# Kernel optimization log

Hardware: AMD Instinct MI355X
Metric: run time of the kernel (lower is better)

The kernel has to match this reference:

```python
import jax, jax.numpy as jnp
import numpy as np

EPS = 1e-5
GROUPS = 16


def _deform_conv_gn(input, offset, mask, weight, bias, gamma, beta):
    # Modulated deformable conv v2 (k=3, stride=1, pad=1) + GroupNorm(16).
    B, C, H, W = input.shape
    Co = weight.shape[0]
    K = 9
    # kernel taps relative to center (pad=1 cancels the -1 origin shift)
    ky = jnp.repeat(jnp.arange(3) - 1, 3).astype(input.dtype)   # [9]
    kx = jnp.tile(jnp.arange(3) - 1, 3).astype(input.dtype)     # [9]
    off = offset.reshape(B, K, 2, H, W)                          # (dy, dx) per tap
    dy, dx = off[:, :, 0], off[:, :, 1]                          # [B,9,H,W]
    y = jnp.arange(H, dtype=input.dtype)[None, None, :, None] + ky[None, :, None, None] + dy
    x = jnp.arange(W, dtype=input.dtype)[None, None, None, :] + kx[None, :, None, None] + dx
    y0 = jnp.floor(y)
    x0 = jnp.floor(x)
    flat = input.reshape(B, C, H * W)

    def corner(yc, xc):
        # zero-padded bilinear corner gather -> [B,C,9,H,W]
        valid = ((yc >= 0) & (yc < H) & (xc >= 0) & (xc < W)).astype(input.dtype)
        yi = jnp.clip(yc, 0, H - 1).astype(jnp.int32)
        xi = jnp.clip(xc, 0, W - 1).astype(jnp.int32)
        idx = (yi * W + xi).reshape(B, -1)
        g = jax.vmap(lambda im, ix: jnp.take(im, ix, axis=1))(flat, idx)
        return g.reshape(B, C, K, H, W) * valid[:, None]

    wy1 = y - y0
    wx1 = x - x0
    wy0 = 1.0 - wy1
    wx0 = 1.0 - wx1
    val = (corner(y0, x0) * (wy0 * wx0)[:, None]
           + corner(y0, x0 + 1.0) * (wy0 * wx1)[:, None]
           + corner(y0 + 1.0, x0) * (wy1 * wx0)[:, None]
           + corner(y0 + 1.0, x0 + 1.0) * (wy1 * wx1)[:, None])
    cols = val * mask[:, None]                                   # modulation [B,C,9,H,W]
    out = jnp.einsum('bckhw,ock->bohw', cols, weight.reshape(Co, C, K))
    out = out + bias[None, :, None, None]
    # GroupNorm(16)
    g = out.reshape(B, GROUPS, Co // GROUPS, H, W)
    mu = g.mean(axis=(2, 3, 4), keepdims=True)
    var = g.var(axis=(2, 3, 4), keepdims=True)
    g = (g - mu) * jax.lax.rsqrt(var + EPS)
    return g.reshape(B, Co, H, W) * gamma[None, :, None, None] + beta[None, :, None, None]


def setup_inputs() -> dict:
    key = jax.random.key(0)
    k1, k2, k3, k4 = jax.random.split(key, 4)
    B, C, Co, H, W = 4, 256, 256, 64, 64
    return {
        'input': jax.random.normal(k1, (B, C, H, W), dtype=jnp.float32),
        'offset': jax.random.normal(k2, (B, 18, H, W), dtype=jnp.float32),
        'mask': jax.random.uniform(k3, (B, 9, H, W), dtype=jnp.float32),
        'weight': jax.random.normal(k4, (Co, C, 3, 3), dtype=jnp.float32) * 0.02,
        'bias': jnp.zeros((Co,), dtype=jnp.float32),
        'gamma': jnp.ones((Co,), dtype=jnp.float32),
        'beta': jnp.zeros((Co,), dtype=jnp.float32),
    }


def reference(input, offset, mask, weight, bias, gamma, beta):
    return _deform_conv_gn(input, offset, mask, weight, bias, gamma, beta)
```

## Files before the change

### kernel.cpp

```cpp
#include <hip/hip_runtime.h>

typedef __attribute__((ext_vector_type(8))) short short8;
typedef __attribute__((ext_vector_type(4))) float f32x4;

#define Bsz 4
#define Cin 256
#define Cout 256
#define Hh 64
#define Ww 64
#define HW 4096
#define NG 16
#define EPSV 1e-5f

#define SPAN 12
#define ROWB 4112

#define OFF_IN   0
#define SZ_IN    (SPAN * ROWB)
#define OFF_COL  49344
#define SZ_COL   (9 * 2048)
#define OFF_CTL  67776
#define SMEM_BYTES 67792

static __device__ __forceinline__ unsigned f2bf(float f) {
    unsigned u = __float_as_uint(f);
    return (u + 0x7fffu + ((u >> 16) & 1u)) >> 16;
}

static __device__ __forceinline__ float2 ld8(const float* p) {
    float2 v;
    __builtin_memcpy(&v, p, 8);
    return v;
}

#define BLO(u) __uint_as_float((u) << 16)
#define BHI(u) __uint_as_float((u) & 0xffff0000u)

__launch_bounds__(512)
__global__ void prep_kernel(const float* __restrict__ in,
                            const float* __restrict__ w,
                            unsigned* __restrict__ inT,
                            ushort* __restrict__ wtb,
                            float* __restrict__ stats) {
    const int t  = threadIdx.x;
    const int bx = blockIdx.x;
    if (bx < 256) {
        const int b = bx >> 6, y = bx & 63;
        const int x = t & 63, w8 = t >> 6;
        const float* src = in + (size_t)b * 256 * HW + y * 64 + x;
        unsigned* dst = inT + ((size_t)(b * 64 + y) * 128) * 64 + x;
#pragma unroll
        for (int it = 0; it < 16; it++) {
            const int pr = w8 + it * 8;
            const float a0 = src[(size_t)(2 * pr) * HW];
            const float a1 = src[(size_t)(2 * pr + 1) * HW];
            dst[(size_t)pr * 64] = f2bf(a0) | (f2bf(a1) << 16);
        }
        return;
    }
    if (bx == 256 && t < 128) stats[t] = 0.f;
    const int i = (bx - 256) * 512 + t;
    if (i >= 72 * 256 * 32) return;
    const int cl = i & 31;
    const int o  = (i >> 5) & 255;
    const int ks = i >> 13;
    const int c  = ((ks & 7) << 5) | cl;
    const int kk = ks >> 3;
    wtb[i] = (ushort)f2bf(w[((size_t)o * Cin + c) * 9 + kk]);
}

__launch_bounds__(512, 4)
__global__ void dcn_kernel(const float* __restrict__ in,
                           const unsigned* __restrict__ inT,
                           const float* __restrict__ offs,
                           const float* __restrict__ mask,
                           const ushort* __restrict__ wtb,
                           const float* __restrict__ bias,
                           float* __restrict__ out,
                           float* __restrict__ stats) {
    extern __shared__ char smem[];
    ushort* col  = (ushort*)(smem + OFF_COL);
    int*    s_ctl = (int*)(smem + OFF_CTL);

    const int t  = threadIdx.x;
    const int bx = blockIdx.x;
    const int q  = bx & 7, r = bx >> 3;
    const int b  = q >> 1;
    const int h  = ((q & 1) << 5) | (r >> 1);
    const int wb = (r & 1) << 5;
    const int lane = t & 63;
    const int wv   = t >> 6;
    const int quad = lane >> 4;
    const int l15  = lane & 15;
    const int px   = lane & 31;
    const int hi   = lane >> 5;
    const int proff = (2 * wv + hi) * 256;
    const int pp   = wb + px;
    const int cslot = ((px >> 4) << 9) | ((wv >> 1) << 7) | ((px & 15) << 3) |
                      ((wv & 1) << 2) | (hi << 1);

    if (t < 2) s_ctl[t] = (t == 0) ? 64 : -1;
    __syncthreads();

    const float* ob = offs + (size_t)b * 18 * HW + h * Ww + pp;
    const float* mb = mask + (size_t)b * 9 * HW + h * Ww + pp;
    int ryc0[9], ryc1[9], rxb[9];
    float4 tw4[9];
    int my_min = 64, my_max = -1;
#pragma unroll
    for (int k = 0; k < 9; k++) {
        const float dy = ob[(2 * k) * HW];
        const float dx = ob[(2 * k + 1) * HW];
        const float m  = mb[k * HW];
        const float y = (float)h + (float)(k / 3 - 1) + dy;
        const float x = (float)pp + (float)(k % 3 - 1) + dx;
        const float y0f = floorf(y), x0f = floorf(x);
        const float ly = y - y0f, lx = x - x0f;
        const float hy = 1.f - ly, hx = 1.f - lx;
        const int y0 = (int)y0f, x0 = (int)x0f;
        const int yc0 = min(max(y0, 0), 63);
        const int yc1 = min(max(y0 + 1, 0), 63);
        const int xb  = min(max(x0, 0), 62);
        float ax = 0.f, ay = 0.f;
        if (x0 == xb) {
            ax = hx;
            ay = lx;
        } else if (x0 < xb) {
            ax = (x0 + 1 == 0) ? lx : 0.f;
        } else {
            ay = (x0 == 63) ? hx : 0.f;
        }
        const float w0 = (y0 >= 0 && y0 < 64) ? m * hy : 0.f;
        const float w1 = (y0 + 1 >= 0 && y0 + 1 < 64) ? m * ly : 0.f;
        ryc0[k] = yc0; ryc1[k] = yc1; rxb[k] = xb;
        tw4[k] = make_float4(w0 * ax, w0 * ay, w1 * ax, w1 * ay);
        my_min = min(my_min, yc0);
        my_max = max(my_max, yc1);
    }
#pragma unroll
    for (int off = 32; off; off >>= 1) {
        my_min = min(my_min, __shfl_xor(my_min, off));
        my_max = max(my_max, __shfl_xor(my_max, off));
    }
    if (lane == 0) {
        atomicMin(&s_ctl[0], my_min);
        atomicMax(&s_ctl[1], my_max);
    }
    __syncthreads();

    const int ymin = s_ctl[0];
    const bool use_lds = (s_ctl[1] - ymin + 1) <= SPAN;

    unsigned tad[9];
#pragma unroll
    for (int k = 0; k < 9; k++) {
        const unsigned r0 = (unsigned)((ryc0[k] - ymin) * ROWB + rxb[k] * 4);
        const unsigned r1 = (unsigned)((ryc1[k] - ymin) * ROWB + rxb[k] * 4);
        tad[k] = (r0 & 0xffffu) | (r1 << 16);
    }

    f32x4 acc[2][2];
#pragma unroll
    for (int i = 0; i < 2; i++)
#pragma unroll
        for (int nt = 0; nt < 2; nt++) acc[i][nt] = (f32x4){0.f, 0.f, 0.f, 0.f};

    const float* inb = in + (size_t)b * Cin * HW;

#define STAGE(cc)                                                              \
    {                                                                          \
        _Pragma("unroll")                                                      \
        for (int i = 0; i < 6; i++) {                                          \
            const int g = wv * 6 + i;                                          \
            const int rr = g >> 2, seg = g & 3;                                \
            const int row = min(ymin + rr, 63);                                \
            const unsigned* src = inT +                                        \
                ((size_t)(b * 64 + row) * 128 + (cc) * 16) * 64 +              \
                seg * 256 + lane * 4;                                          \
            __builtin_amdgcn_global_load_lds(                                  \
                (const __attribute__((address_space(1))) void*)src,            \
                (__attribute__((address_space(3))) void*)(smem + OFF_IN +      \
                    rr * ROWB + seg * 1024),                                   \
                16, 0, 0);                                                     \
        }                                                                      \
    }

#define GATHER_PUB_L(kk)                                                   \
    {                                                                      \
        const unsigned ad = tad[kk];                                       \
        const float4 tw = tw4[kk];                                         \
        const char* bp = smem + OFF_IN + proff;                            \
        const float2 f0 = ld8((const float*)(bp + (ad & 0xffffu)));        \
        const float2 f1 = ld8((const float*)(bp + (ad >> 16)));            \
        const unsigned u00 = __float_as_uint(f0.x);                        \
        const unsigned u01 = __float_as_uint(f0.y);                        \
        const unsigned u10 = __float_as_uint(f1.x);                        \
        const unsigned u11 = __float_as_uint(f1.y);                        \
        const float v0 = tw.x * BLO(u00) + tw.y * BLO(u01) +               \
                         tw.z * BLO(u10) + tw.w * BLO(u11);                \
        const float v1 = tw.x * BHI(u00) + tw.y * BHI(u01) +               \
                         tw.z * BHI(u10) + tw.w * BHI(u11);                \
        *(unsigned*)&col[(kk) * 1024 + cslot] = f2bf(v0) | (f2bf(v1) << 16); \
    }

#define FRAGS_MFMA(ks, kk)                                                     \
    {                                                                          \
        const ushort* wp =                                                     \
            wtb + ((size_t)((ks) * 256 + wv * 32 + l15)) * 32 + quad * 8;      \
        const short8 a0 = *(const short8*)wp;                                  \
        const short8 a1 = *(const short8*)(wp + 16 * 32);                      \
        short8 bfr[2];                                                         \
        _Pragma("unroll")                                                      \
        for (int nt = 0; nt < 2; nt++)                                         \
            bfr[nt] = *(const short8*)&col[(kk) * 1024 + nt * 512 +            \
                                           quad * 128 + l15 * 8];              \
        _Pragma("unroll")                                                      \
        for (int nt = 0; nt < 2; nt++) {                                       \
            acc[0][nt] = __builtin_amdgcn_mfma_f32_16x16x32_bf16(              \
                a0, bfr[nt], acc[0][nt], 0, 0, 0);                             \
            acc[1][nt] = __builtin_amdgcn_mfma_f32_16x16x32_bf16(              \
                a1, bfr[nt], acc[1][nt], 0, 0, 0);                             \
        }                                                                      \
    }

    if (use_lds) {
        STAGE(0);
        __syncthreads();
#pragma unroll 1
        for (int cc = 0; cc < 8; cc++) {
#pragma unroll
            for (int kk = 0; kk < 9; kk++) GATHER_PUB_L(kk);
            __syncthreads();
            if (cc < 7) STAGE(cc + 1);
#pragma unroll 3
            for (int kk = 0; kk < 9; kk++) FRAGS_MFMA(kk * 8 + cc, kk);
            __syncthreads();
        }
    } else {
#pragma unroll 1
        for (int cc = 0; cc < 8; cc++) {
#pragma unroll 1
            for (int kk = 0; kk < 9; kk++) {
                const float dy = ob[(2 * kk) * HW];
                const float dx = ob[(2 * kk + 1) * HW];
                const float m  = mb[kk * HW];
                const float y = (float)h + (float)(kk / 3 - 1) + dy;
                const float x = (float)pp + (float)(kk % 3 - 1) + dx;
                const float y0f = floorf(y), x0f = floorf(x);
                const float ly = y - y0f, lx = x - x0f;
                const float hy = 1.f - ly, hx = 1.f - lx;
                const int y0 = (int)y0f, x0 = (int)x0f;
                const int yc0 = min(max(y0, 0), 63);
                const int yc1 = min(max(y0 + 1, 0), 63);
                const int xb  = min(max(x0, 0), 62);
                float ax = 0.f, ay = 0.f;
                if (x0 == xb)      { ax = hx; ay = lx; }
                else if (x0 < xb)  { ax = (x0 + 1 == 0) ? lx : 0.f; }
                else               { ay = (x0 == 63) ? hx : 0.f; }
                const float w0 = (y0 >= 0 && y0 < 64) ? m * hy : 0.f;
                const float w1 = (y0 + 1 >= 0 && y0 + 1 < 64) ? m * ly : 0.f;
                const int adx = yc0 * 64 + xb, ady = yc1 * 64 + xb;
                const float* cb = inb + (size_t)(cc * 32 + wv * 4 + hi * 2) * HW;
                float vv[2];
#pragma unroll
                for (int j = 0; j < 2; j++) {
                    const float* pl = cb + j * HW;
                    const float2 g0 = ld8(pl + adx);
                    const float2 g1 = ld8(pl + ady);
                    vv[j] = (w0 * ax) * g0.x + (w0 * ay) * g0.y +
                            (w1 * ax) * g1.x + (w1 * ay) * g1.y;
                }
                *(unsigned*)&col[kk * 1024 + cslot] =
                    f2bf(vv[0]) | (f2bf(vv[1]) << 16);
            }
            __syncthreads();
#pragma unroll 3
            for (int kk = 0; kk < 9; kk++) FRAGS_MFMA(kk * 8 + cc, kk);
            __syncthreads();
        }
    }
#undef STAGE
#undef GATHER_PUB_L
#undef FRAGS_MFMA

    float gs[2], gq[2];
#pragma unroll
    for (int i = 0; i < 2; i++) {
        float s = 0.f, qq = 0.f;
        const int ob2 = wv * 32 + i * 16 + quad * 4;
#pragma unroll
        for (int reg = 0; reg < 4; reg++) {
            const int o = ob2 + reg;
            const float bv = bias[o];
            float* op = out + ((size_t)(b * 256 + o)) * HW + h * Ww + wb + l15;
#pragma unroll
            for (int nt = 0; nt < 2; nt++) {
                const float v = acc[i][nt][reg] + bv;
                op[nt * 16] = v;
                s += v;
                qq += v * v;
            }
        }
        gs[i] = s; gq[i] = qq;
    }
#pragma unroll
    for (int off = 32; off; off >>= 1) {
        gs[0] += __shfl_xor(gs[0], off);
        gq[0] += __shfl_xor(gq[0], off);
        gs[1] += __shfl_xor(gs[1], off);
        gq[1] += __shfl_xor(gq[1], off);
    }
    if (lane == 0) {
#pragma unroll
        for (int i = 0; i < 2; i++) {
            const int g = wv * 2 + i;
            atomicAdd(&stats[((size_t)b * NG + g) * 2],     gs[i]);
            atomicAdd(&stats[((size_t)b * NG + g) * 2 + 1], gq[i]);
        }
    }
}

__global__ void gn_apply_kernel(float* __restrict__ x, const float* __restrict__ stats,
                                const float* __restrict__ gamma,
                                const float* __restrict__ beta) {
    const int i = blockIdx.x * 256 + threadIdx.x;
    const int plane = i >> 10;
    const int o = plane & 255;
    const int bg = plane >> 4;
    const float s = stats[bg * 2], q = stats[bg * 2 + 1];
    const float inv_n = 1.f / 65536.f;
    const float mu = s * inv_n;
    const float var = q * inv_n - mu * mu;
    const float rs = rsqrtf(var + EPSV);
    const float ga = gamma[o] * rs;
    const float be = beta[o] - mu * ga;
    float4 v = ((float4*)x)[i];
    v.x = v.x * ga + be;
    v.y = v.y * ga + be;
    v.z = v.z * ga + be;
    v.w = v.w * ga + be;
    ((float4*)x)[i] = v;
}

extern "C" void kernel_launch(void* const* d_in, const int* in_sizes, int n_in,
                              void* d_out, int out_size, void* d_ws, size_t ws_size,
                              hipStream_t stream) {
    const float* input  = (const float*)d_in[0];
    const float* offset = (const float*)d_in[1];
    const float* maskp  = (const float*)d_in[2];
    const float* weight = (const float*)d_in[3];
    const float* bias   = (const float*)d_in[4];
    const float* gamma  = (const float*)d_in[5];
    const float* beta   = (const float*)d_in[6];
    float* out = (float*)d_out;

    ushort* wtb  = (ushort*)d_ws;
    float* stats = (float*)((char*)d_ws + (size_t)Cout * Cin * 9 * sizeof(ushort));
    unsigned* inT = (unsigned*)((char*)d_ws + 1180160);

    static int attr_done = 0;
    if (!attr_done) {
        hipFuncSetAttribute((const void*)dcn_kernel,
                            hipFuncAttributeMaxDynamicSharedMemorySize, SMEM_BYTES);
        attr_done = 1;
    }

    hipLaunchKernelGGL(prep_kernel, dim3(256 + 1152), dim3(512), 0, stream,
                       input, weight, inT, wtb, stats);
    hipLaunchKernelGGL(dcn_kernel, dim3(Bsz * Hh * 2), dim3(512), SMEM_BYTES, stream,
                       input, inT, offset, maskp, wtb, bias, out, stats);
    hipLaunchKernelGGL(gn_apply_kernel, dim3((Bsz * Cout * HW / 4) / 256), dim3(256), 0,
                       stream, out, stats, gamma, beta);
}
```

Baseline: 195.4 us.

## Fuse prep, deformable conv and GroupNorm into one cooperative grid-synced kernel

Replaces the three launches (prep transpose/weight conversion, DCN+stats, GN apply) with a single cooperative kernel of 512 blocks that uses grid-wide syncs between phases. The conv results are kept in registers so GroupNorm is applied without writing and re-reading the pre-norm output. This removes two launch gaps and one full round trip of the output through global memory. In exchange it adds grid barriers, requires all blocks to be co-resident (launch bounds of 4 blocks per CU), and may put register pressure on the accumulator path. It falls back to the old three-kernel path if cooperative launch is unavailable.

New measurement: 196.1 us. No clear change (+0.4%).

```diff
diff --git a/kernel.cpp b/kernel.cpp
--- a/kernel.cpp
+++ b/kernel.cpp
@@ -1,4 +1,7 @@
 #include <hip/hip_runtime.h>
+#include <hip/hip_cooperative_groups.h>
+
+namespace cg = cooperative_groups;
 
 typedef __attribute__((ext_vector_type(8))) short short8;
 typedef __attribute__((ext_vector_type(4))) float f32x4;
@@ -35,6 +38,305 @@
 
 #define BLO(u) __uint_as_float((u) << 16)
 #define BHI(u) __uint_as_float((u) & 0xffff0000u)
+
+#define STAGE(cc)                                                              \
+    {                                                                          \
+        _Pragma("unroll")                                                      \
+        for (int i = 0; i < 6; i++) {                                          \
+            const int g = wv * 6 + i;                                          \
+            const int rr = g >> 2, seg = g & 3;                                \
+            const int row = min(ymin + rr, 63);                                \
+            const unsigned* src = inT +                                        \
+                ((size_t)(b * 64 + row) * 128 + (cc) * 16) * 64 +              \
+                seg * 256 + lane * 4;                                          \
+            __builtin_amdgcn_global_load_lds(                                  \
+                (const __attribute__((address_space(1))) void*)src,            \
+                (__attribute__((address_space(3))) void*)(smem + OFF_IN +      \
+                    rr * ROWB + seg * 1024),                                   \
+                16, 0, 0);                                                     \
+        }                                                                      \
+    }
+
+#define GATHER_PUB_L(kk)                                                   \
+    {                                                                      \
+        const unsigned ad = tad[kk];                                       \
+        const float4 tw = tw4[kk];                                         \
+        const char* bp = smem + OFF_IN + proff;                            \
+        const float2 f0 = ld8((const float*)(bp + (ad & 0xffffu)));        \
+        const float2 f1 = ld8((const float*)(bp + (ad >> 16)));            \
+        const unsigned u00 = __float_as_uint(f0.x);                        \
+        const unsigned u01 = __float_as_uint(f0.y);                        \
+        const unsigned u10 = __float_as_uint(f1.x);                        \
+        const unsigned u11 = __float_as_uint(f1.y);                        \
+        const float v0 = tw.x * BLO(u00) + tw.y * BLO(u01) +               \
+                         tw.z * BLO(u10) + tw.w * BLO(u11);                \
+        const float v1 = tw.x * BHI(u00) + tw.y * BHI(u01) +               \
+                         tw.z * BHI(u10) + tw.w * BHI(u11);                \
+        *(unsigned*)&col[(kk) * 1024 + cslot] = f2bf(v0) | (f2bf(v1) << 16); \
+    }
+
+#define FRAGS_MFMA(ks, kk)                                                     \
+    {                                                                          \
+        const ushort* wp =                                                     \
+            wtb + ((size_t)((ks) * 256 + wv * 32 + l15)) * 32 + quad * 8;      \
+        const short8 a0 = *(const short8*)wp;                                  \
+        const short8 a1 = *(const short8*)(wp + 16 * 32);                      \
+        short8 bfr[2];                                                         \
+        _Pragma("unroll")                                                      \
+        for (int nt = 0; nt < 2; nt++)                                         \
+            bfr[nt] = *(const short8*)&col[(kk) * 1024 + nt * 512 +            \
+                                           quad * 128 + l15 * 8];              \
+        _Pragma("unroll")                                                      \
+        for (int nt = 0; nt < 2; nt++) {                                       \
+            acc[0][nt] = __builtin_amdgcn_mfma_f32_16x16x32_bf16(              \
+                a0, bfr[nt], acc[0][nt], 0, 0, 0);                             \
+            acc[1][nt] = __builtin_amdgcn_mfma_f32_16x16x32_bf16(              \
+                a1, bfr[nt], acc[1][nt], 0, 0, 0);                             \
+        }                                                                      \
+    }
+
+#define DCN_BODY(WRITE_OUT)                                                    \
+    if (t < 2) s_ctl[t] = (t == 0) ? 64 : -1;                                  \
+    __syncthreads();                                                           \
+    const float* ob = offs + (size_t)b * 18 * HW + h * Ww + pp;                \
+    const float* mb = mask + (size_t)b * 9 * HW + h * Ww + pp;                 \
+    int ryc0[9], ryc1[9], rxb[9];                                              \
+    float4 tw4[9];                                                             \
+    int my_min = 64, my_max = -1;                                              \
+    _Pragma("unroll")                                                          \
+    for (int k = 0; k < 9; k++) {                                              \
+        const float dy = ob[(2 * k) * HW];                                     \
+        const float dx = ob[(2 * k + 1) * HW];                                 \
+        const float m  = mb[k * HW];                                           \
+        const float y = (float)h + (float)(k / 3 - 1) + dy;                    \
+        const float x = (float)pp + (float)(k % 3 - 1) + dx;                   \
+        const float y0f = floorf(y), x0f = floorf(x);                          \
+        const float ly = y - y0f, lx = x - x0f;                                \
+        const float hy = 1.f - ly, hx = 1.f - lx;                              \
+        const int y0 = (int)y0f, x0 = (int)x0f;                                \
+        const int yc0 = min(max(y0, 0), 63);                                   \
+        const int yc1 = min(max(y0 + 1, 0), 63);                               \
+        const int xb  = min(max(x0, 0), 62);                                   \
+        float ax = 0.f, ay = 0.f;                                              \
+        if (x0 == xb)      { ax = hx; ay = lx; }                               \
+        else if (x0 < xb)  { ax = (x0 + 1 == 0) ? lx : 0.f; }                  \
+        else               { ay = (x0 == 63) ? hx : 0.f; }                     \
+        const float w0 = (y0 >= 0 && y0 < 64) ? m * hy : 0.f;                  \
+        const float w1 = (y0 + 1 >= 0 && y0 + 1 < 64) ? m * ly : 0.f;          \
+        ryc0[k] = yc0; ryc1[k] = yc1; rxb[k] = xb;                             \
+        tw4[k] = make_float4(w0 * ax, w0 * ay, w1 * ax, w1 * ay);              \
+        my_min = min(my_min, yc0);                                             \
+        my_max = max(my_max, yc1);                                             \
+    }                                                                          \
+    _Pragma("unroll")                                                          \
+    for (int off = 32; off; off >>= 1) {                                       \
+        my_min = min(my_min, __shfl_xor(my_min, off));                         \
+        my_max = max(my_max, __shfl_xor(my_max, off));                         \
+    }                                                                          \
+    if (lane == 0) {                                                           \
+        atomicMin(&s_ctl[0], my_min);                                          \
+        atomicMax(&s_ctl[1], my_max);                                          \
+    }                                                                          \
+    __syncthreads();                                                           \
+    const int ymin = s_ctl[0];                                                 \
+    const bool use_lds2 = (s_ctl[1] - ymin + 1) <= SPAN;                       \
+    unsigned tad[9];                                                           \
+    _Pragma("unroll")                                                          \
+    for (int k = 0; k < 9; k++) {                                              \
+        const unsigned r0 = (unsigned)((ryc0[k] - ymin) * ROWB + rxb[k] * 4);  \
+        const unsigned r1 = (unsigned)((ryc1[k] - ymin) * ROWB + rxb[k] * 4);  \
+        tad[k] = (r0 & 0xffffu) | (r1 << 16);                                  \
+    }                                                                          \
+    f32x4 acc[2][2];                                                           \
+    _Pragma("unroll")                                                          \
+    for (int i = 0; i < 2; i++)                                                \
+        _Pragma("unroll")                                                      \
+        for (int nt = 0; nt < 2; nt++) acc[i][nt] = (f32x4){0.f,0.f,0.f,0.f};  \
+    const float* inb = in + (size_t)b * Cin * HW;                              \
+    if (use_lds2) {                                                            \
+        STAGE(0);                                                              \
+        __syncthreads();                                                       \
+        _Pragma("unroll 1")                                                    \
+        for (int cc = 0; cc < 8; cc++) {                                       \
+            _Pragma("unroll")                                                  \
+            for (int kk = 0; kk < 9; kk++) GATHER_PUB_L(kk);                   \
+            __syncthreads();                                                   \
+            if (cc < 7) STAGE(cc + 1);                                         \
+            _Pragma("unroll 3")                                                \
+            for (int kk = 0; kk < 9; kk++) FRAGS_MFMA(kk * 8 + cc, kk);        \
+            __syncthreads();                                                   \
+        }                                                                      \
+    } else {                                                                   \
+        _Pragma("unroll 1")                                                    \
+        for (int cc = 0; cc < 8; cc++) {                                       \
+            _Pragma("unroll 1")                                                \
+            for (int kk = 0; kk < 9; kk++) {                                   \
+                const float dy = ob[(2 * kk) * HW];                            \
+                const float dx = ob[(2 * kk + 1) * HW];                        \
+                const float m  = mb[kk * HW];                                  \
+                const float y = (float)h + (float)(kk / 3 - 1) + dy;           \
+                const float x = (float)pp + (float)(kk % 3 - 1) + dx;          \
+                const float y0f = floorf(y), x0f = floorf(x);                  \
+                const float ly = y - y0f, lx = x - x0f;                        \
+                const float hy = 1.f - ly, hx = 1.f - lx;                      \
+                const int y0 = (int)y0f, x0 = (int)x0f;                        \
+                const int yc0 = min(max(y0, 0), 63);                           \
+                const int yc1 = min(max(y0 + 1, 0), 63);                       \
+                const int xb  = min(max(x0, 0), 62);                           \
+                float ax = 0.f, ay = 0.f;                                      \
+                if (x0 == xb)      { ax = hx; ay = lx; }                       \
+                else if (x0 < xb)  { ax = (x0 + 1 == 0) ? lx : 0.f; }          \
+                else               { ay = (x0 == 63) ? hx : 0.f; }             \
+                const float w0 = (y0 >= 0 && y0 < 64) ? m * hy : 0.f;          \
+                const float w1 = (y0 + 1 >= 0 && y0 + 1 < 64) ? m * ly : 0.f;  \
+                const int adx = yc0 * 64 + xb, ady = yc1 * 64 + xb;            \
+                const float* cb = inb + (size_t)(cc*32 + wv*4 + hi*2) * HW;    \
+                float vv[2];                                                   \
+                _Pragma("unroll")                                              \
+                for (int j = 0; j < 2; j++) {                                  \
+                    const float* pl = cb + j * HW;                             \
+                    const float2 g0 = ld8(pl + adx);                           \
+                    const float2 g1 = ld8(pl + ady);                           \
+                    vv[j] = (w0 * ax) * g0.x + (w0 * ay) * g0.y +              \
+                            (w1 * ax) * g1.x + (w1 * ay) * g1.y;               \
+                }                                                              \
+                *(unsigned*)&col[kk * 1024 + cslot] =                          \
+                    f2bf(vv[0]) | (f2bf(vv[1]) << 16);                         \
+            }                                                                  \
+            __syncthreads();                                                   \
+            _Pragma("unroll 3")                                                \
+            for (int kk = 0; kk < 9; kk++) FRAGS_MFMA(kk * 8 + cc, kk);        \
+            __syncthreads();                                                   \
+        }                                                                      \
+    }                                                                          \
+    float gs[2], gq[2];                                                        \
+    _Pragma("unroll")                                                          \
+    for (int i = 0; i < 2; i++) {                                              \
+        float s = 0.f, qq = 0.f;                                               \
+        const int ob2 = wv * 32 + i * 16 + quad * 4;                           \
+        _Pragma("unroll")                                                      \
+        for (int reg = 0; reg < 4; reg++) {                                    \
+            const int o = ob2 + reg;                                           \
+            const float bv = bias[o];                                          \
+            float* op = out + ((size_t)(b * 256 + o)) * HW + h * Ww + wb + l15;\
+            _Pragma("unroll")                                                  \
+            for (int nt = 0; nt < 2; nt++) {                                   \
+                const float v = acc[i][nt][reg] + bv;                          \
+                acc[i][nt][reg] = v;                                           \
+                if (WRITE_OUT) op[nt * 16] = v;                                \
+                s += v;                                                        \
+                qq += v * v;                                                   \
+            }                                                                  \
+        }                                                                      \
+        gs[i] = s; gq[i] = qq;                                                 \
+    }                                                                          \
+    _Pragma("unroll")                                                          \
+    for (int off = 32; off; off >>= 1) {                                       \
+        gs[0] += __shfl_xor(gs[0], off);                                       \
+        gq[0] += __shfl_xor(gq[0], off);                                       \
+        gs[1] += __shfl_xor(gs[1], off);                                       \
+        gq[1] += __shfl_xor(gq[1], off);                                       \
+    }                                                                          \
+    if (lane == 0) {                                                           \
+        _Pragma("unroll")                                                      \
+        for (int i = 0; i < 2; i++) {                                          \
+            const int g = wv * 2 + i;                                          \
+            atomicAdd(&stats[((size_t)b * NG + g) * 2],     gs[i]);            \
+            atomicAdd(&stats[((size_t)b * NG + g) * 2 + 1], gq[i]);            \
+        }                                                                      \
+    }
+
+__launch_bounds__(512, 4)
+__global__ void fused_kernel(const float* __restrict__ in,
+                             const float* __restrict__ offs,
+                             const float* __restrict__ mask,
+                             const float* __restrict__ w,
+                             const float* __restrict__ bias,
+                             const float* __restrict__ gamma,
+                             const float* __restrict__ beta,
+                             float* __restrict__ out,
+                             unsigned* __restrict__ inT,
+                             ushort* __restrict__ wtb,
+                             float* __restrict__ stats) {
+    extern __shared__ char smem[];
+    ushort* col  = (ushort*)(smem + OFF_COL);
+    int*    s_ctl = (int*)(smem + OFF_CTL);
+
+    const int t  = threadIdx.x;
+    const int bx = blockIdx.x;
+
+    {
+        const int pb = bx >> 7;
+        const int py = (bx >> 1) & 63;
+        const int ph = bx & 1;
+        const int x = t & 63, w8 = t >> 6;
+        const float* src = in + (size_t)pb * 256 * HW + py * 64 + x;
+        unsigned* dst = inT + ((size_t)(pb * 64 + py) * 128) * 64 + x;
+#pragma unroll
+        for (int it = 0; it < 8; it++) {
+            const int pr = ph * 64 + w8 + it * 8;
+            const float a0 = src[(size_t)(2 * pr) * HW];
+            const float a1 = src[(size_t)(2 * pr + 1) * HW];
+            dst[(size_t)pr * 64] = f2bf(a0) | (f2bf(a1) << 16);
+        }
+#pragma unroll
+        for (int j = 0; j < 3; j++) {
+            const int l = j * 512 + t;
+            if (l < 1152) {
+                const int i = bx * 1152 + l;
+                const int cl = i & 31;
+                const int o  = (i >> 5) & 255;
+                const int ks = i >> 13;
+                const int c  = ((ks & 7) << 5) | cl;
+                const int kk = ks >> 3;
+                wtb[i] = (ushort)f2bf(w[((size_t)o * Cin + c) * 9 + kk]);
+            }
+        }
+        if (bx == 0 && t < 128) stats[t] = 0.f;
+    }
+    cg::this_grid().sync();
+
+    const int q  = bx & 7, r = bx >> 3;
+    const int b  = q >> 1;
+    const int h  = ((q & 1) << 5) | (r >> 1);
+    const int wb = (r & 1) << 5;
+    const int lane = t & 63;
+    const int wv   = t >> 6;
+    const int quad = lane >> 4;
+    const int l15  = lane & 15;
+    const int px   = lane & 31;
+    const int hi   = lane >> 5;
+    const int proff = (2 * wv + hi) * 256;
+    const int pp   = wb + px;
+    const int cslot = ((px >> 4) << 9) | ((wv >> 1) << 7) | ((px & 15) << 3) |
+                      ((wv & 1) << 2) | (hi << 1);
+
+    DCN_BODY(0)
+
+    cg::this_grid().sync();
+
+    const float inv_n = 1.f / 65536.f;
+#pragma unroll
+    for (int i = 0; i < 2; i++) {
+        const int g = wv * 2 + i;
+        const float ssum = stats[((size_t)b * NG + g) * 2];
+        const float sq   = stats[((size_t)b * NG + g) * 2 + 1];
+        const float mu  = ssum * inv_n;
+        const float var = sq * inv_n - mu * mu;
+        const float rs  = rsqrtf(var + EPSV);
+        const int ob2 = wv * 32 + i * 16 + quad * 4;
+#pragma unroll
+        for (int reg = 0; reg < 4; reg++) {
+            const int o = ob2 + reg;
+            const float ga = gamma[o] * rs;
+            const float be = beta[o] - mu * ga;
+            float* op = out + ((size_t)(b * 256 + o)) * HW + h * Ww + wb + l15;
+#pragma unroll
+            for (int nt = 0; nt < 2; nt++)
+                op[nt * 16] = acc[i][nt][reg] * ga + be;
+        }
+    }
+}
 
 __launch_bounds__(512)
 __global__ void prep_kernel(const float* __restrict__ in,
@@ -99,226 +401,13 @@
     const int cslot = ((px >> 4) << 9) | ((wv >> 1) << 7) | ((px & 15) << 3) |
                       ((wv & 1) << 2) | (hi << 1);
 
-    if (t < 2) s_ctl[t] = (t == 0) ? 64 : -1;
-    __syncthreads();
-
-    const float* ob = offs + (size_t)b * 18 * HW + h * Ww + pp;
-    const float* mb = mask + (size_t)b * 9 * HW + h * Ww + pp;
-    int ryc0[9], ryc1[9], rxb[9];
-    float4 tw4[9];
-    int my_min = 64, my_max = -1;
-#pragma unroll
-    for (int k = 0; k < 9; k++) {
-        const float dy = ob[(2 * k) * HW];
-        const float dx = ob[(2 * k + 1) * HW];
-        const float m  = mb[k * HW];
-        const float y = (float)h + (float)(k / 3 - 1) + dy;
-        const float x = (float)pp + (float)(k % 3 - 1) + dx;
-        const float y0f = floorf(y), x0f = floorf(x);
-        const float ly = y - y0f, lx = x - x0f;
-        const float hy = 1.f - ly, hx = 1.f - lx;
-        const int y0 = (int)y0f, x0 = (int)x0f;
-        const int yc0 = min(max(y0, 0), 63);
-        const int yc1 = min(max(y0 + 1, 0), 63);
-        const int xb  = min(max(x0, 0), 62);
-        float ax = 0.f, ay = 0.f;
-        if (x0 == xb) {
-            ax = hx;
-            ay = lx;
-        } else if (x0 < xb) {
-            ax = (x0 + 1 == 0) ? lx : 0.f;
-        } else {
-            ay = (x0 == 63) ? hx : 0.f;
-        }
-        const float w0 = (y0 >= 0 && y0 < 64) ? m * hy : 0.f;
-        const float w1 = (y0 + 1 >= 0 && y0 + 1 < 64) ? m * ly : 0.f;
-        ryc0[k] = yc0; ryc1[k] = yc1; rxb[k] = xb;
-        tw4[k] = make_float4(w0 * ax, w0 * ay, w1 * ax, w1 * ay);
-        my_min = min(my_min, yc0);
-        my_max = max(my_max, yc1);
-    }
-#pragma unroll
-    for (int off = 32; off; off >>= 1) {
-        my_min = min(my_min, __shfl_xor(my_min, off));
-        my_max = max(my_max, __shfl_xor(my_max, off));
-    }
-    if (lane == 0) {
-        atomicMin(&s_ctl[0], my_min);
-        atomicMax(&s_ctl[1], my_max);
-    }
-    __syncthreads();
-
-    const int ymin = s_ctl[0];
-    const bool use_lds = (s_ctl[1] - ymin + 1) <= SPAN;
-
-    unsigned tad[9];
-#pragma unroll
-    for (int k = 0; k < 9; k++) {
-        const unsigned r0 = (unsigned)((ryc0[k] - ymin) * ROWB + rxb[k] * 4);
-        const unsigned r1 = (unsigned)((ryc1[k] - ymin) * ROWB + rxb[k] * 4);
-        tad[k] = (r0 & 0xffffu) | (r1 << 16);
-    }
-
-    f32x4 acc[2][2];
-#pragma unroll
-    for (int i = 0; i < 2; i++)
-#pragma unroll
-        for (int nt = 0; nt < 2; nt++) acc[i][nt] = (f32x4){0.f, 0.f, 0.f, 0.f};
-
-    const float* inb = in + (size_t)b * Cin * HW;
-
-#define STAGE(cc)                                                              \
-    {                                                                          \
-        _Pragma("unroll")                                                      \
-        for (int i = 0; i < 6; i++) {                                          \
-            const int g = wv * 6 + i;                                          \
-            const int rr = g >> 2, seg = g & 3;                                \
-            const int row = min(ymin + rr, 63);                                \
-            const unsigned* src = inT +                                        \
-                ((size_t)(b * 64 + row) * 128 + (cc) * 16) * 64 +              \
-                seg * 256 + lane * 4;                                          \
-            __builtin_amdgcn_global_load_lds(                                  \
-                (const __attribute__((address_space(1))) void*)src,            \
-                (__attribute__((address_space(3))) void*)(smem + OFF_IN +      \
-                    rr * ROWB + seg * 1024),                                   \
-                16, 0, 0);                                                     \
-        }                                                                      \
-    }
-
-#define GATHER_PUB_L(kk)                                                   \
-    {                                                                      \
-        const unsigned ad = tad[kk];                                       \
-        const float4 tw = tw4[kk];                                         \
-        const char* bp = smem + OFF_IN + proff;                            \
-        const float2 f0 = ld8((const float*)(bp + (ad & 0xffffu)));        \
-        const float2 f1 = ld8((const float*)(bp + (ad >> 16)));            \
-        const unsigned u00 = __float_as_uint(f0.x);                        \
-        const unsigned u01 = __float_as_uint(f0.y);                        \
-        const unsigned u10 = __float_as_uint(f1.x);                        \
-        const unsigned u11 = __float_as_uint(f1.y);                        \
-        const float v0 = tw.x * BLO(u00) + tw.y * BLO(u01) +               \
-                         tw.z * BLO(u10) + tw.w * BLO(u11);                \
-        const float v1 = tw.x * BHI(u00) + tw.y * BHI(u01) +               \
-                         tw.z * BHI(u10) + tw.w * BHI(u11);                \
-        *(unsigned*)&col[(kk) * 1024 + cslot] = f2bf(v0) | (f2bf(v1) << 16); \
-    }
-
-#define FRAGS_MFMA(ks, kk)                                                     \
-    {                                                                          \
-        const ushort* wp =                                                     \
-            wtb + ((size_t)((ks) * 256 + wv * 32 + l15)) * 32 + quad * 8;      \
-        const short8 a0 = *(const short8*)wp;                                  \
-        const short8 a1 = *(const short8*)(wp + 16 * 32);                      \
-        short8 bfr[2];                                                         \
-        _Pragma("unroll")                                                      \
-        for (int nt = 0; nt < 2; nt++)                                         \
-            bfr[nt] = *(const short8*)&col[(kk) * 1024 + nt * 512 +            \
-                                           quad * 128 + l15 * 8];              \
-        _Pragma("unroll")                                                      \
-        for (int nt = 0; nt < 2; nt++) {                                       \
-            acc[0][nt] = __builtin_amdgcn_mfma_f32_16x16x32_bf16(              \
-                a0, bfr[nt], acc[0][nt], 0, 0, 0);                             \
-            acc[1][nt] = __builtin_amdgcn_mfma_f32_16x16x32_bf16(              \
-                a1, bfr[nt], acc[1][nt], 0, 0, 0);                             \
-        }                                                                      \
-    }
-
-    if (use_lds) {
-        STAGE(0);
-        __syncthreads();
-#pragma unroll 1
-        for (int cc = 0; cc < 8; cc++) {
-#pragma unroll
-            for (int kk = 0; kk < 9; kk++) GATHER_PUB_L(kk);
-            __syncthreads();
-            if (cc < 7) STAGE(cc + 1);
-#pragma unroll 3
-            for (int kk = 0; kk < 9; kk++) FRAGS_MFMA(kk * 8 + cc, kk);
-            __syncthreads();
-        }
-    } else {
-#pragma unroll 1
-        for (int cc = 0; cc < 8; cc++) {
-#pragma unroll 1
-            for (int kk = 0; kk < 9; kk++) {
-                const float dy = ob[(2 * kk) * HW];
-                const float dx = ob[(2 * kk + 1) * HW];
-                const float m  = mb[kk * HW];
-                const float y = (float)h + (float)(kk / 3 - 1) + dy;
-                const float x = (float)pp + (float)(kk % 3 - 1) + dx;
-                const float y0f = floorf(y), x0f = floorf(x);
-                const float ly = y - y0f, lx = x - x0f;
-                const float hy = 1.f - ly, hx = 1.f - lx;
-                const int y0 = (int)y0f, x0 = (int)x0f;
-                const int yc0 = min(max(y0, 0), 63);
-                const int yc1 = min(max(y0 + 1, 0), 63);
-                const int xb  = min(max(x0, 0), 62);
-                float ax = 0.f, ay = 0.f;
-                if (x0 == xb)      { ax = hx; ay = lx; }
-                else if (x0 < xb)  { ax = (x0 + 1 == 0) ? lx : 0.f; }
-                else               { ay = (x0 == 63) ? hx : 0.f; }
-                const float w0 = (y0 >= 0 && y0 < 64) ? m * hy : 0.f;
-                const float w1 = (y0 + 1 >= 0 && y0 + 1 < 64) ? m * ly : 0.f;
-                const int adx = yc0 * 64 + xb, ady = yc1 * 64 + xb;
-                const float* cb = inb + (size_t)(cc * 32 + wv * 4 + hi * 2) * HW;
-                float vv[2];
-#pragma unroll
-                for (int j = 0; j < 2; j++) {
-                    const float* pl = cb + j * HW;
-                    const float2 g0 = ld8(pl + adx);
-                    const float2 g1 = ld8(pl + ady);
-                    vv[j] = (w0 * ax) * g0.x + (w0 * ay) * g0.y +
-                            (w1 * ax) * g1.x + (w1 * ay) * g1.y;
-                }
-                *(unsigned*)&col[kk * 1024 + cslot] =
-                    f2bf(vv[0]) | (f2bf(vv[1]) << 16);
-            }
-            __syncthreads();
-#pragma unroll 3
-            for (int kk = 0; kk < 9; kk++) FRAGS_MFMA(kk * 8 + cc, kk);
-            __syncthreads();
-        }
-    }
+    DCN_BODY(1)
+}
+
 #undef STAGE
 #undef GATHER_PUB_L
 #undef FRAGS_MFMA
-
-    float gs[2], gq[2];
-#pragma unroll
-    for (int i = 0; i < 2; i++) {
-        float s = 0.f, qq = 0.f;
-        const int ob2 = wv * 32 + i * 16 + quad * 4;
-#pragma unroll
-        for (int reg = 0; reg < 4; reg++) {
-            const int o = ob2 + reg;
-            const float bv = bias[o];
-            float* op = out + ((size_t)(b * 256 + o)) * HW + h * Ww + wb + l15;
-#pragma unroll
-            for (int nt = 0; nt < 2; nt++) {
-                const float v = acc[i][nt][reg] + bv;
-                op[nt * 16] = v;
-                s += v;
-                qq += v * v;
-            }
-        }
-        gs[i] = s; gq[i] = qq;
-    }
-#pragma unroll
-    for (int off = 32; off; off >>= 1) {
-        gs[0] += __shfl_xor(gs[0], off);
-        gq[0] += __shfl_xor(gq[0], off);
-        gs[1] += __shfl_xor(gs[1], off);
-        gq[1] += __shfl_xor(gq[1], off);
-    }
-    if (lane == 0) {
-#pragma unroll
-        for (int i = 0; i < 2; i++) {
-            const int g = wv * 2 + i;
-            atomicAdd(&stats[((size_t)b * NG + g) * 2],     gs[i]);
-            atomicAdd(&stats[((size_t)b * NG + g) * 2 + 1], gq[i]);
-        }
-    }
-}
+#undef DCN_BODY
 
 __global__ void gn_apply_kernel(float* __restrict__ x, const float* __restrict__ stats,
                                 const float* __restrict__ gamma,
@@ -358,11 +447,28 @@
     float* stats = (float*)((char*)d_ws + (size_t)Cout * Cin * 9 * sizeof(ushort));
     unsigned* inT = (unsigned*)((char*)d_ws + 1180160);
 
-    static int attr_done = 0;
-    if (!attr_done) {
+    static int mode = -1;
+    if (mode < 0) {
+        hipFuncSetAttribute((const void*)fused_kernel,
+                            hipFuncAttributeMaxDynamicSharedMemorySize, SMEM_BYTES);
         hipFuncSetAttribute((const void*)dcn_kernel,
                             hipFuncAttributeMaxDynamicSharedMemorySize, SMEM_BYTES);
-        attr_done = 1;
+        int dev = 0, coop = 0;
+        hipGetDevice(&dev);
+        hipDeviceGetAttribute(&coop, hipDeviceAttributeCooperativeLaunch, dev);
+        mode = coop ? 1 : 0;
+    }
+
+    if (mode == 1) {
+        void* kargs[] = {(void*)&input, (void*)&offset, (void*)&maskp,
+                         (void*)&weight, (void*)&bias, (void*)&gamma,
+                         (void*)&beta, (void*)&out, (void*)&inT,
+                         (void*)&wtb, (void*)&stats};
+        hipError_t e = hipLaunchCooperativeKernel(
+            (const void*)fused_kernel, dim3(512), dim3(512), kargs,
+            SMEM_BYTES, stream);
+        if (e == hipSuccess) return;
+        mode = 0;
     }
 
     hipLaunchKernelGGL(prep_kernel, dim3(256 + 1152), dim3(512), 0, stream,
```
